# Performance work log

Measured on AMD Instinct MI355X. Metric: run time of the kernel, lower is better.

Reference implementation:

```python
import jax, jax.numpy as jnp
import numpy as np

CHANNELS = 128
HEADS = 4
R = 2
LAMBDA = 0.1


def setup_inputs() -> dict:
    key = jax.random.key(0)
    k1, k2 = jax.random.split(key)
    x = jax.random.normal(k1, (1, CHANNELS, 32, 32, 32), dtype=jnp.float32)
    # 1x1x1 Conv3d weight [3C, C] (trailing unit spatial dims dropped), fan-in scaled
    w_qkv = jax.random.normal(k2, (3 * CHANNELS, CHANNELS), dtype=jnp.float32) * (CHANNELS ** -0.5)
    return {"x": x, "w_qkv": w_qkv}


def reference(x, w_qkv):
    head_dim = CHANNELS // HEADS          # 32
    d_half = head_dim // 2                # 16
    scale = head_dim ** -0.5
    # AvgPool3d(kernel_size=1, stride=R) == strided subsampling
    xs = x[:, :, ::R, ::R, ::R]
    B, C, H, W, Z = xs.shape
    N = H * W * Z                          # 4096 tokens
    # 1x1x1 conv == pointwise channel matmul, then group channels heads-major
    qkv = jnp.einsum('oc,bchwz->bohwz', w_qkv, xs).reshape(B, HEADS, 3 * head_dim, N)
    q, k, v = jnp.split(qkv, 3, axis=2)    # each [B, h, head_dim, N]
    q1, q2 = q[:, :, :d_half, :], q[:, :, d_half:, :]
    k1, k2 = k[:, :, :d_half, :], k[:, :, d_half:, :]
    # two full score matrices [B, h, N, N] (differential attention)
    attn1 = jnp.einsum('bhdn,bhdm->bhnm', q1, k1) * scale
    attn2 = jnp.einsum('bhdn,bhdm->bhnm', q2, k2) * scale
    diff_attn = jax.nn.softmax(attn1, axis=-1) - LAMBDA * jax.nn.softmax(attn2, axis=-1)
    out = jnp.einsum('bhnm,bhdm->bhnd', diff_attn, v)  # [B, h, N, head_dim]
    # faithful to torch .view(B, -1, H, W, Z) on contiguous (h, N, head_dim) layout
    return out.reshape(B, C, H, W, Z)
```

## Files before the change

### kernel.cpp

```cpp
#include <hip/hip_runtime.h>

#define N_TOK 4096
#define NH    4

typedef __attribute__((ext_vector_type(8))) short bf16x8;
typedef __attribute__((ext_vector_type(4))) short bf16x4;
typedef __attribute__((ext_vector_type(4))) float f32x4;

static constexpr float SCALE   = 0.17677669529663687f;
static constexpr float QSCALE  = 0.25503632254435463f;
static constexpr float LAMBDA_ = 0.1f;
#define PSTRIDE 2112

__device__ __forceinline__ unsigned short bf_rne(float f) {
    unsigned u = __float_as_uint(f);
    u += 0x7FFF + ((u >> 16) & 1);
    return (unsigned short)(u >> 16);
}

__global__ __launch_bounds__(256) void qkv_kernel(
    const float* __restrict__ x, const float* __restrict__ wsrc,
    unsigned short* __restrict__ qA, unsigned short* __restrict__ kB,
    unsigned short* __restrict__ vT)
{
    __shared__ __align__(16) float xf[16][132];
    __shared__ __align__(16) unsigned short xbh[16 * 136];
    __shared__ __align__(16) unsigned short xbl[16 * 136];
    __shared__ __align__(16) unsigned short qsh[2][16][64];
    __shared__ __align__(16) unsigned short ksh[2][16][64];
    __shared__ __align__(16) unsigned short vsh[2][32][16];

    const int t  = threadIdx.x;
    const int tg = blockIdx.x >> 1;
    const int rh = blockIdx.x & 1;
    const int n0 = tg * 16;
    const int nh = n0 >> 8, nw = (n0 >> 4) & 15;
    const int xbase = nh * 2048 + nw * 64;

    #pragma unroll
    for (int k = 0; k < 4; ++k) {
        int idx = t + k * 256;
        int pair = idx & 7, ch = idx >> 3;
        float4 f4 = *(const float4*)&x[(size_t)ch * 32768 + xbase + pair * 4];
        xf[pair * 2][ch]     = f4.x;
        xf[pair * 2 + 1][ch] = f4.z;
    }
    __syncthreads();
    #pragma unroll
    for (int k = 0; k < 8; ++k) {
        int idx = t + k * 256;
        int tok = idx & 15, ch = idx >> 4;
        float f = xf[tok][ch];
        unsigned u = __float_as_uint(f);
        float lo = f - __uint_as_float(u & 0xFFFF0000u);
        xbh[tok * 136 + ch] = (unsigned short)(u >> 16);
        xbl[tok * 136 + ch] = (unsigned short)(__float_as_uint(lo) >> 16);
    }
    __syncthreads();

    const int lane = t & 63;
    const int m    = lane & 15;
    const int quad = lane >> 4;
    const int w    = t >> 6;

    bf16x8 Bh[4], Bl[4];
    #pragma unroll
    for (int s = 0; s < 4; ++s) {
        Bh[s] = *(const bf16x8*)&xbh[m * 136 + s * 32 + quad * 8];
        Bl[s] = *(const bf16x8*)&xbl[m * 136 + s * 32 + quad * 8];
    }

    #pragma unroll
    for (int rt = 0; rt < 3; ++rt) {
        const int R0 = rh * 192 + w * 48 + rt * 16;
        const int row = R0 + m;
        const int rr_row = row % 96;
        const float sc = (rr_row < 32) ? QSCALE : 1.0f;
        const float* wp = wsrc + (size_t)row * 128;
        bf16x8 Ah[4], Al[4];
        #pragma unroll
        for (int s = 0; s < 4; ++s) {
            float4 f0 = *(const float4*)(wp + s * 32 + quad * 8);
            float4 f1 = *(const float4*)(wp + s * 32 + quad * 8 + 4);
            float fv[8] = {f0.x, f0.y, f0.z, f0.w, f1.x, f1.y, f1.z, f1.w};
            #pragma unroll
            for (int j = 0; j < 8; ++j) {
                float f = fv[j] * sc;
                unsigned u = __float_as_uint(f);
                float lo = f - __uint_as_float(u & 0xFFFF0000u);
                Ah[s][j] = (short)(unsigned short)(u >> 16);
                Al[s][j] = (short)(unsigned short)(__float_as_uint(lo) >> 16);
            }
        }
        f32x4 C = {0, 0, 0, 0};
        #pragma unroll
        for (int s = 0; s < 4; ++s) {
            C = __builtin_amdgcn_mfma_f32_16x16x32_bf16(Ah[s], Bh[s], C, 0, 0, 0);
            C = __builtin_amdgcn_mfma_f32_16x16x32_bf16(Al[s], Bh[s], C, 0, 0, 0);
            C = __builtin_amdgcn_mfma_f32_16x16x32_bf16(Ah[s], Bl[s], C, 0, 0, 0);
        }
        #pragma unroll
        for (int i = 0; i < 4; ++i) {
            int R  = R0 + quad * 4 + i;
            int hh = R / 96;
            int rr = R - hh * 96;
            int hl = hh & 1;
            float f = C[i];
            if (rr < 64) {
                unsigned u = __float_as_uint(f);
                float lo = f - __uint_as_float(u & 0xFFFF0000u);
                unsigned short hi16 = (unsigned short)(u >> 16);
                unsigned short lo16 = (unsigned short)(__float_as_uint(lo) >> 16);
                int part = (rr & 31) >> 4, d = rr & 15;
                if (rr < 32) {
                    qsh[hl][m][part * 32 + d]      = hi16;
                    qsh[hl][m][part * 32 + d + 16] = lo16;
                } else {
                    ksh[hl][m][part * 32 + d]      = hi16;
                    ksh[hl][m][part * 32 + d + 16] = lo16;
                }
            } else {
                vsh[hl][rr - 64][m] = bf_rne(f);
            }
        }
    }
    __syncthreads();

    {
        int rec = t >> 3, g = t & 7;
        int hl  = rec >> 4, i = rec & 15;
        int hh  = rh * 2 + hl;
        int n   = n0 + i;
        size_t qbase = ((size_t)hh * N_TOK + n) * 64 + g * 8;
        *(uint4*)(qA + qbase) = *(const uint4*)&qsh[hl][i][g * 8];

        int tile = n >> 6, ml = n & 63;
        int kh2 = ml >> 5, mlb = (ml >> 4) & 1, mm = ml & 15;
        int f = mlb * 2 + (g >> 2), qd = g & 3;
        size_t koff = (size_t)hh * 262144 + (size_t)tile * 4096
                    + ((kh2 * 4 + f) * 64 + qd * 16 + mm) * 8;
        *(uint4*)(kB + koff) = *(const uint4*)&ksh[hl][i][g * 8];
    }
    if (t < 128) {
        int hl = t >> 6, d = (t >> 1) & 31, half = t & 1;
        int hh = rh * 2 + hl;
        int kb = (n0 >> 3) + half;
        int tile = kb >> 3, kbl = kb & 7;
        int kh2 = kbl >> 2;
        int vf  = ((kbl >> 1) & 1) * 2 + (d >> 4);
        int mm  = d & 15;
        size_t vbase = (size_t)hh * 131072 + (size_t)tile * 2048 + (kh2 * 4 + vf) * 256;
        int q0 = (kbl & 1) << 1;
        *(uint2*)(vT + vbase + (q0 * 16 + mm) * 4)       = *(const uint2*)&vsh[hl][d][half * 8];
        *(uint2*)(vT + vbase + ((q0 + 1) * 16 + mm) * 4) = *(const uint2*)&vsh[hl][d][half * 8 + 4];
    }
}

__global__ __launch_bounds__(256, 4) void flash_kernel(
    const unsigned short* __restrict__ qA, const unsigned short* __restrict__ kB,
    const unsigned short* __restrict__ vT, float* __restrict__ parts)
{
    __shared__ float Obuf[2][2][16][33];
    __shared__ float lbuf[2][2][16];

    const int t    = threadIdx.x;
    const int w    = t >> 6;
    const int lane = t & 63;
    const int m    = lane & 15;
    const int quad = lane >> 4;
    const int ks   = blockIdx.x & 1;
    const int qt   = (blockIdx.x >> 1) & 127;
    const int h    = blockIdx.x >> 8;
    const int qtile = w >> 1;
    const int kh    = w & 1;
    const int qbase = qt * 32;

    for (int i = t; i < 2112; i += 256) ((float*)Obuf)[i] = 0.f;
    if (t < 64) ((float*)lbuf)[t] = 0.f;
    __syncthreads();

    const unsigned short* qrec = qA + (size_t)(h * N_TOK + qbase + qtile * 16 + m) * 64;
    const bf16x8 zz = {0,0,0,0,0,0,0,0};
    bf16x8 Bq1h = *(const bf16x8*)(qrec + (quad & 1) * 8);
    bf16x8 Bq2h = *(const bf16x8*)(qrec + 32 + (quad & 1) * 8);
    bf16x8 Bq1l = (quad < 2) ? *(const bf16x8*)(qrec + 16 + quad * 8) : zz;
    bf16x8 Bq2l = (quad < 2) ? *(const bf16x8*)(qrec + 48 + quad * 8) : zz;

    f32x4 O1a = {0,0,0,0}, O1b = {0,0,0,0}, O2a = {0,0,0,0}, O2b = {0,0,0,0};
    float l1 = 0.f, l2 = 0.f;

    const unsigned short* kt = kB + (size_t)h * 262144 + (size_t)ks * 131072;
    const unsigned short* vt = vT + (size_t)h * 131072 + (size_t)ks * 65536;
    const int kcb = kh * 2048 + lane * 8;
    const int vcb = kh * 1024 + lane * 4;

    bf16x8 Ka0, Ka1, Ka2, Ka3, Kb0, Kb1, Kb2, Kb3;
    bf16x4 Va0, Va1, Va2, Va3, Vb0, Vb1, Vb2, Vb3;

#define LOADSET(K0, K1, K2, K3, V0, V1, V2, V3, TILE)                          \
    {                                                                          \
        const unsigned short* kp = kt + (size_t)(TILE) * 4096 + kcb;           \
        const unsigned short* vp = vt + (size_t)(TILE) * 2048 + vcb;           \
        K0 = *(const bf16x8*)(kp);                                             \
        K1 = *(const bf16x8*)(kp + 512);                                       \
        K2 = *(const bf16x8*)(kp + 1024);                                      \
        K3 = *(const bf16x8*)(kp + 1536);                                      \
        V0 = *(const bf16x4*)(vp);                                             \
        V1 = *(const bf16x4*)(vp + 256);                                       \
        V2 = *(const bf16x4*)(vp + 512);                                       \
        V3 = *(const bf16x4*)(vp + 768);                                       \
    }

    auto compute = [&](bf16x8 K1_0, bf16x8 K2_0, bf16x8 K1_1, bf16x8 K2_1,
                       bf16x4 V00, bf16x4 V10, bf16x4 V01, bf16x4 V11) {
        __builtin_amdgcn_s_setprio(1);
        f32x4 sA1 = {0,0,0,0}, sA2 = {0,0,0,0};
        f32x4 sB1 = {0,0,0,0}, sB2 = {0,0,0,0};
        sA1 = __builtin_amdgcn_mfma_f32_16x16x32_bf16(K1_0, Bq1h, sA1, 0, 0, 0);
        sB1 = __builtin_amdgcn_mfma_f32_16x16x32_bf16(K1_1, Bq1h, sB1, 0, 0, 0);
        sA1 = __builtin_amdgcn_mfma_f32_16x16x32_bf16(K1_0, Bq1l, sA1, 0, 0, 0);
        sB1 = __builtin_amdgcn_mfma_f32_16x16x32_bf16(K1_1, Bq1l, sB1, 0, 0, 0);
        sA2 = __builtin_amdgcn_mfma_f32_16x16x32_bf16(K2_0, Bq2h, sA2, 0, 0, 0);
        sB2 = __builtin_amdgcn_mfma_f32_16x16x32_bf16(K2_1, Bq2h, sB2, 0, 0, 0);
        sA2 = __builtin_amdgcn_mfma_f32_16x16x32_bf16(K2_0, Bq2l, sA2, 0, 0, 0);
        sB2 = __builtin_amdgcn_mfma_f32_16x16x32_bf16(K2_1, Bq2l, sB2, 0, 0, 0);

        float pa0 = __builtin_amdgcn_exp2f(sA1[0]), pa1 = __builtin_amdgcn_exp2f(sA1[1]);
        float pa2 = __builtin_amdgcn_exp2f(sA1[2]), pa3 = __builtin_amdgcn_exp2f(sA1[3]);
        float pb0 = __builtin_amdgcn_exp2f(sB1[0]), pb1 = __builtin_amdgcn_exp2f(sB1[1]);
        float pb2 = __builtin_amdgcn_exp2f(sB1[2]), pb3 = __builtin_amdgcn_exp2f(sB1[3]);
        float qa0 = __builtin_amdgcn_exp2f(sA2[0]), qa1 = __builtin_amdgcn_exp2f(sA2[1]);
        float qa2 = __builtin_amdgcn_exp2f(sA2[2]), qa3 = __builtin_amdgcn_exp2f(sA2[3]);
        float qb0 = __builtin_amdgcn_exp2f(sB2[0]), qb1 = __builtin_amdgcn_exp2f(sB2[1]);
        float qb2 = __builtin_amdgcn_exp2f(sB2[2]), qb3 = __builtin_amdgcn_exp2f(sB2[3]);
        l1 += (pa0 + pa1) + (pa2 + pa3) + (pb0 + pb1) + (pb2 + pb3);
        l2 += (qa0 + qa1) + (qa2 + qa3) + (qb0 + qb1) + (qb2 + qb3);
        union { unsigned u[2]; bf16x4 v; } cA1, cB1, cA2, cB2;
        cA1.u[0] = __builtin_amdgcn_perm(__float_as_uint(pa1), __float_as_uint(pa0), 0x07060302u);
        cA1.u[1] = __builtin_amdgcn_perm(__float_as_uint(pa3), __float_as_uint(pa2), 0x07060302u);
        cB1.u[0] = __builtin_amdgcn_perm(__float_as_uint(pb1), __float_as_uint(pb0), 0x07060302u);
        cB1.u[1] = __builtin_amdgcn_perm(__float_as_uint(pb3), __float_as_uint(pb2), 0x07060302u);
        cA2.u[0] = __builtin_amdgcn_perm(__float_as_uint(qa1), __float_as_uint(qa0), 0x07060302u);
        cA2.u[1] = __builtin_amdgcn_perm(__float_as_uint(qa3), __float_as_uint(qa2), 0x07060302u);
        cB2.u[0] = __builtin_amdgcn_perm(__float_as_uint(qb1), __float_as_uint(qb0), 0x07060302u);
        cB2.u[1] = __builtin_amdgcn_perm(__float_as_uint(qb3), __float_as_uint(qb2), 0x07060302u);

        O1a = __builtin_amdgcn_mfma_f32_16x16x16bf16_1k(cA1.v, V00, O1a, 0, 0, 0);
        O1b = __builtin_amdgcn_mfma_f32_16x16x16bf16_1k(cA1.v, V10, O1b, 0, 0, 0);
        O2a = __builtin_amdgcn_mfma_f32_16x16x16bf16_1k(cA2.v, V00, O2a, 0, 0, 0);
        O2b = __builtin_amdgcn_mfma_f32_16x16x16bf16_1k(cA2.v, V10, O2b, 0, 0, 0);
        O1a = __builtin_amdgcn_mfma_f32_16x16x16bf16_1k(cB1.v, V01, O1a, 0, 0, 0);
        O1b = __builtin_amdgcn_mfma_f32_16x16x16bf16_1k(cB1.v, V11, O1b, 0, 0, 0);
        O2a = __builtin_amdgcn_mfma_f32_16x16x16bf16_1k(cB2.v, V01, O2a, 0, 0, 0);
        O2b = __builtin_amdgcn_mfma_f32_16x16x16bf16_1k(cB2.v, V11, O2b, 0, 0, 0);
        __builtin_amdgcn_s_setprio(0);
    };

    LOADSET(Ka0, Ka1, Ka2, Ka3, Va0, Va1, Va2, Va3, 0);
    for (int tile = 0; tile < 32; tile += 2) {
        LOADSET(Kb0, Kb1, Kb2, Kb3, Vb0, Vb1, Vb2, Vb3, tile + 1);
        compute(Ka0, Ka1, Ka2, Ka3, Va0, Va1, Va2, Va3);
        if (tile + 2 < 32)
            LOADSET(Ka0, Ka1, Ka2, Ka3, Va0, Va1, Va2, Va3, tile + 2);
        compute(Kb0, Kb1, Kb2, Kb3, Vb0, Vb1, Vb2, Vb3);
    }
#undef LOADSET

    l1 += __shfl_xor(l1, 16, 64); l1 += __shfl_xor(l1, 32, 64);
    l2 += __shfl_xor(l2, 16, 64); l2 += __shfl_xor(l2, 32, 64);
    if (lane < 16) {
        atomicAdd(&lbuf[qtile][0][m], l1);
        atomicAdd(&lbuf[qtile][1][m], l2);
    }
    #pragma unroll
    for (int i = 0; i < 4; ++i) {
        int r = quad * 4 + i;
        atomicAdd(&Obuf[qtile][0][r][m],      O1a[i]);
        atomicAdd(&Obuf[qtile][0][r][16 + m], O1b[i]);
        atomicAdd(&Obuf[qtile][1][r][m],      O2a[i]);
        atomicAdd(&Obuf[qtile][1][r][16 + m], O2b[i]);
    }
    __syncthreads();

    float* dst = parts + (size_t)((h * 128 + qt) * 2 + ks) * PSTRIDE;
    for (int i = t; i < 1024; i += 256) {
        int r = i >> 5, d = i & 31;
        int qtl = r >> 4, rl = r & 15;
        dst[i]        = Obuf[qtl][0][rl][d];
        dst[1024 + i] = Obuf[qtl][1][rl][d];
    }
    if (t < 32) {
        int qtl = t >> 4, rl = t & 15;
        dst[2048 + t] = lbuf[qtl][0][rl];
        dst[2080 + t] = lbuf[qtl][1][rl];
    }
}

__global__ __launch_bounds__(256) void merge_kernel(
    const float* __restrict__ parts, float* __restrict__ out)
{
    int idx = blockIdx.x * 256 + threadIdx.x;
    int d4 = (idx & 7) * 4;
    int row = idx >> 3;
    int h = row >> 12, n = row & 4095;
    int qt = n >> 5, r = n & 31;
    const float* p0 = parts + (size_t)((h * 128 + qt) * 2) * PSTRIDE;
    const float* p1 = p0 + PSTRIDE;
    float4 a1 = *(const float4*)(p0 + r * 32 + d4);
    float4 b1 = *(const float4*)(p1 + r * 32 + d4);
    float4 a2 = *(const float4*)(p0 + 1024 + r * 32 + d4);
    float4 b2 = *(const float4*)(p1 + 1024 + r * 32 + d4);
    float l1 = p0[2048 + r] + p1[2048 + r];
    float l2 = p0[2080 + r] + p1[2080 + r];
    float4 o;
    o.x = (a1.x + b1.x) / l1 - LAMBDA_ * ((a2.x + b2.x) / l2);
    o.y = (a1.y + b1.y) / l1 - LAMBDA_ * ((a2.y + b2.y) / l2);
    o.z = (a1.z + b1.z) / l1 - LAMBDA_ * ((a2.z + b2.z) / l2);
    o.w = (a1.w + b1.w) / l1 - LAMBDA_ * ((a2.w + b2.w) / l2);
    *(float4*)(out + (size_t)idx * 4) = o;
}

extern "C" void kernel_launch(void* const* d_in, const int* in_sizes, int n_in,
                              void* d_out, int out_size, void* d_ws, size_t ws_size,
                              hipStream_t stream) {
    const float* x = (const float*)d_in[0];
    const float* w = (const float*)d_in[1];
    float* out = (float*)d_out;

    unsigned short* qA = (unsigned short*)d_ws;
    unsigned short* kB = qA + (size_t)NH * N_TOK * 64;
    unsigned short* vT = kB + (size_t)NH * N_TOK * 64;
    float* parts = (float*)(vT + (size_t)NH * 32 * N_TOK);

    qkv_kernel<<<512, 256, 0, stream>>>(x, w, qA, kB, vT);
    flash_kernel<<<1024, 256, 0, stream>>>(qA, kB, vT, parts);
    merge_kernel<<<512, 256, 0, stream>>>(parts, out);
}
```

Baseline: 120.7 us.

## Software-pipeline QK^T of the next tile with softmax and PV of the current

Splits the per-tile work into separate QK^T and exp/PV phases and staggers them. The score MFMAs for tile i+1 are issued before the exp2, pack and PV MFMAs of tile i, with K loads running one further tile ahead of V loads. The goal is to hide MFMA result latency and the exp/pack VALU work behind independent matrix ops. In exchange it keeps two sets of score accumulators live, and the launch bound no longer requests 4 blocks per CU. The compiler can therefore use more registers, which may lower occupancy.

```diff
diff --git a/kernel.cpp b/kernel.cpp
--- a/kernel.cpp
+++ b/kernel.cpp
@@ -156,7 +156,7 @@
     }
 }
 
-__global__ __launch_bounds__(256, 4) void flash_kernel(
+__global__ __launch_bounds__(256) void flash_kernel(
     const unsigned short* __restrict__ qA, const unsigned short* __restrict__ kB,
     const unsigned short* __restrict__ vT, float* __restrict__ parts)
 {
@@ -194,77 +194,90 @@
     const int kcb = kh * 2048 + lane * 8;
     const int vcb = kh * 1024 + lane * 4;
 
-    bf16x8 Ka0, Ka1, Ka2, Ka3, Kb0, Kb1, Kb2, Kb3;
-    bf16x4 Va0, Va1, Va2, Va3, Vb0, Vb1, Vb2, Vb3;
-
-#define LOADSET(K0, K1, K2, K3, V0, V1, V2, V3, TILE)                          \
-    {                                                                          \
+    bf16x8 K00, K01, K02, K03, K10, K11, K12, K13;
+    bf16x4 V00_, V01_, V02_, V03_, V10_, V11_, V12_, V13_;
+    f32x4 S0A1, S0B1, S0A2, S0B2, S1A1, S1B1, S1A2, S1B2;
+
+#define LOADK(KS, TILE) {                                                      \
         const unsigned short* kp = kt + (size_t)(TILE) * 4096 + kcb;           \
+        KS##0 = *(const bf16x8*)(kp);                                          \
+        KS##1 = *(const bf16x8*)(kp + 512);                                    \
+        KS##2 = *(const bf16x8*)(kp + 1024);                                   \
+        KS##3 = *(const bf16x8*)(kp + 1536);                                   \
+    }
+#define LOADV(VS, TILE) {                                                      \
         const unsigned short* vp = vt + (size_t)(TILE) * 2048 + vcb;           \
-        K0 = *(const bf16x8*)(kp);                                             \
-        K1 = *(const bf16x8*)(kp + 512);                                       \
-        K2 = *(const bf16x8*)(kp + 1024);                                      \
-        K3 = *(const bf16x8*)(kp + 1536);                                      \
-        V0 = *(const bf16x4*)(vp);                                             \
-        V1 = *(const bf16x4*)(vp + 256);                                       \
-        V2 = *(const bf16x4*)(vp + 512);                                       \
-        V3 = *(const bf16x4*)(vp + 768);                                       \
-    }
-
-    auto compute = [&](bf16x8 K1_0, bf16x8 K2_0, bf16x8 K1_1, bf16x8 K2_1,
-                       bf16x4 V00, bf16x4 V10, bf16x4 V01, bf16x4 V11) {
-        __builtin_amdgcn_s_setprio(1);
-        f32x4 sA1 = {0,0,0,0}, sA2 = {0,0,0,0};
-        f32x4 sB1 = {0,0,0,0}, sB2 = {0,0,0,0};
-        sA1 = __builtin_amdgcn_mfma_f32_16x16x32_bf16(K1_0, Bq1h, sA1, 0, 0, 0);
-        sB1 = __builtin_amdgcn_mfma_f32_16x16x32_bf16(K1_1, Bq1h, sB1, 0, 0, 0);
-        sA1 = __builtin_amdgcn_mfma_f32_16x16x32_bf16(K1_0, Bq1l, sA1, 0, 0, 0);
-        sB1 = __builtin_amdgcn_mfma_f32_16x16x32_bf16(K1_1, Bq1l, sB1, 0, 0, 0);
-        sA2 = __builtin_amdgcn_mfma_f32_16x16x32_bf16(K2_0, Bq2h, sA2, 0, 0, 0);
-        sB2 = __builtin_amdgcn_mfma_f32_16x16x32_bf16(K2_1, Bq2h, sB2, 0, 0, 0);
-        sA2 = __builtin_amdgcn_mfma_f32_16x16x32_bf16(K2_0, Bq2l, sA2, 0, 0, 0);
-        sB2 = __builtin_amdgcn_mfma_f32_16x16x32_bf16(K2_1, Bq2l, sB2, 0, 0, 0);
-
-        float pa0 = __builtin_amdgcn_exp2f(sA1[0]), pa1 = __builtin_amdgcn_exp2f(sA1[1]);
-        float pa2 = __builtin_amdgcn_exp2f(sA1[2]), pa3 = __builtin_amdgcn_exp2f(sA1[3]);
-        float pb0 = __builtin_amdgcn_exp2f(sB1[0]), pb1 = __builtin_amdgcn_exp2f(sB1[1]);
-        float pb2 = __builtin_amdgcn_exp2f(sB1[2]), pb3 = __builtin_amdgcn_exp2f(sB1[3]);
-        float qa0 = __builtin_amdgcn_exp2f(sA2[0]), qa1 = __builtin_amdgcn_exp2f(sA2[1]);
-        float qa2 = __builtin_amdgcn_exp2f(sA2[2]), qa3 = __builtin_amdgcn_exp2f(sA2[3]);
-        float qb0 = __builtin_amdgcn_exp2f(sB2[0]), qb1 = __builtin_amdgcn_exp2f(sB2[1]);
-        float qb2 = __builtin_amdgcn_exp2f(sB2[2]), qb3 = __builtin_amdgcn_exp2f(sB2[3]);
-        l1 += (pa0 + pa1) + (pa2 + pa3) + (pb0 + pb1) + (pb2 + pb3);
-        l2 += (qa0 + qa1) + (qa2 + qa3) + (qb0 + qb1) + (qb2 + qb3);
-        union { unsigned u[2]; bf16x4 v; } cA1, cB1, cA2, cB2;
-        cA1.u[0] = __builtin_amdgcn_perm(__float_as_uint(pa1), __float_as_uint(pa0), 0x07060302u);
-        cA1.u[1] = __builtin_amdgcn_perm(__float_as_uint(pa3), __float_as_uint(pa2), 0x07060302u);
-        cB1.u[0] = __builtin_amdgcn_perm(__float_as_uint(pb1), __float_as_uint(pb0), 0x07060302u);
-        cB1.u[1] = __builtin_amdgcn_perm(__float_as_uint(pb3), __float_as_uint(pb2), 0x07060302u);
-        cA2.u[0] = __builtin_amdgcn_perm(__float_as_uint(qa1), __float_as_uint(qa0), 0x07060302u);
-        cA2.u[1] = __builtin_amdgcn_perm(__float_as_uint(qa3), __float_as_uint(qa2), 0x07060302u);
-        cB2.u[0] = __builtin_amdgcn_perm(__float_as_uint(qb1), __float_as_uint(qb0), 0x07060302u);
-        cB2.u[1] = __builtin_amdgcn_perm(__float_as_uint(qb3), __float_as_uint(qb2), 0x07060302u);
-
-        O1a = __builtin_amdgcn_mfma_f32_16x16x16bf16_1k(cA1.v, V00, O1a, 0, 0, 0);
-        O1b = __builtin_amdgcn_mfma_f32_16x16x16bf16_1k(cA1.v, V10, O1b, 0, 0, 0);
-        O2a = __builtin_amdgcn_mfma_f32_16x16x16bf16_1k(cA2.v, V00, O2a, 0, 0, 0);
-        O2b = __builtin_amdgcn_mfma_f32_16x16x16bf16_1k(cA2.v, V10, O2b, 0, 0, 0);
-        O1a = __builtin_amdgcn_mfma_f32_16x16x16bf16_1k(cB1.v, V01, O1a, 0, 0, 0);
-        O1b = __builtin_amdgcn_mfma_f32_16x16x16bf16_1k(cB1.v, V11, O1b, 0, 0, 0);
-        O2a = __builtin_amdgcn_mfma_f32_16x16x16bf16_1k(cB2.v, V01, O2a, 0, 0, 0);
-        O2b = __builtin_amdgcn_mfma_f32_16x16x16bf16_1k(cB2.v, V11, O2b, 0, 0, 0);
-        __builtin_amdgcn_s_setprio(0);
-    };
-
-    LOADSET(Ka0, Ka1, Ka2, Ka3, Va0, Va1, Va2, Va3, 0);
-    for (int tile = 0; tile < 32; tile += 2) {
-        LOADSET(Kb0, Kb1, Kb2, Kb3, Vb0, Vb1, Vb2, Vb3, tile + 1);
-        compute(Ka0, Ka1, Ka2, Ka3, Va0, Va1, Va2, Va3);
-        if (tile + 2 < 32)
-            LOADSET(Ka0, Ka1, Ka2, Ka3, Va0, Va1, Va2, Va3, tile + 2);
-        compute(Kb0, Kb1, Kb2, Kb3, Vb0, Vb1, Vb2, Vb3);
-    }
-#undef LOADSET
+        VS##0_ = *(const bf16x4*)(vp);                                         \
+        VS##1_ = *(const bf16x4*)(vp + 256);                                   \
+        VS##2_ = *(const bf16x4*)(vp + 512);                                   \
+        VS##3_ = *(const bf16x4*)(vp + 768);                                   \
+    }
+#define QKPH(SS, KS) {                                                         \
+        __builtin_amdgcn_s_setprio(1);                                         \
+        SS##A1 = (f32x4){0,0,0,0}; SS##B1 = (f32x4){0,0,0,0};                  \
+        SS##A2 = (f32x4){0,0,0,0}; SS##B2 = (f32x4){0,0,0,0};                  \
+        SS##A1 = __builtin_amdgcn_mfma_f32_16x16x32_bf16(KS##0, Bq1h, SS##A1, 0, 0, 0); \
+        SS##B1 = __builtin_amdgcn_mfma_f32_16x16x32_bf16(KS##2, Bq1h, SS##B1, 0, 0, 0); \
+        SS##A1 = __builtin_amdgcn_mfma_f32_16x16x32_bf16(KS##0, Bq1l, SS##A1, 0, 0, 0); \
+        SS##B1 = __builtin_amdgcn_mfma_f32_16x16x32_bf16(KS##2, Bq1l, SS##B1, 0, 0, 0); \
+        SS##A2 = __builtin_amdgcn_mfma_f32_16x16x32_bf16(KS##1, Bq2h, SS##A2, 0, 0, 0); \
+        SS##B2 = __builtin_amdgcn_mfma_f32_16x16x32_bf16(KS##3, Bq2h, SS##B2, 0, 0, 0); \
+        SS##A2 = __builtin_amdgcn_mfma_f32_16x16x32_bf16(KS##1, Bq2l, SS##A2, 0, 0, 0); \
+        SS##B2 = __builtin_amdgcn_mfma_f32_16x16x32_bf16(KS##3, Bq2l, SS##B2, 0, 0, 0); \
+    }
+#define PVPH(SS, VS) {                                                         \
+        float pa0 = __builtin_amdgcn_exp2f(SS##A1[0]), pa1 = __builtin_amdgcn_exp2f(SS##A1[1]); \
+        float pa2 = __builtin_amdgcn_exp2f(SS##A1[2]), pa3 = __builtin_amdgcn_exp2f(SS##A1[3]); \
+        float pb0 = __builtin_amdgcn_exp2f(SS##B1[0]), pb1 = __builtin_amdgcn_exp2f(SS##B1[1]); \
+        float pb2 = __builtin_amdgcn_exp2f(SS##B1[2]), pb3 = __builtin_amdgcn_exp2f(SS##B1[3]); \
+        float qa0 = __builtin_amdgcn_exp2f(SS##A2[0]), qa1 = __builtin_amdgcn_exp2f(SS##A2[1]); \
+        float qa2 = __builtin_amdgcn_exp2f(SS##A2[2]), qa3 = __builtin_amdgcn_exp2f(SS##A2[3]); \
+        float qb0 = __builtin_amdgcn_exp2f(SS##B2[0]), qb1 = __builtin_amdgcn_exp2f(SS##B2[1]); \
+        float qb2 = __builtin_amdgcn_exp2f(SS##B2[2]), qb3 = __builtin_amdgcn_exp2f(SS##B2[3]); \
+        l1 += (pa0 + pa1) + (pa2 + pa3) + (pb0 + pb1) + (pb2 + pb3);           \
+        l2 += (qa0 + qa1) + (qa2 + qa3) + (qb0 + qb1) + (qb2 + qb3);           \
+        union { unsigned u[2]; bf16x4 v; } cA1, cB1, cA2, cB2;                 \
+        cA1.u[0] = __builtin_amdgcn_perm(__float_as_uint(pa1), __float_as_uint(pa0), 0x07060302u); \
+        cA1.u[1] = __builtin_amdgcn_perm(__float_as_uint(pa3), __float_as_uint(pa2), 0x07060302u); \
+        cB1.u[0] = __builtin_amdgcn_perm(__float_as_uint(pb1), __float_as_uint(pb0), 0x07060302u); \
+        cB1.u[1] = __builtin_amdgcn_perm(__float_as_uint(pb3), __float_as_uint(pb2), 0x07060302u); \
+        cA2.u[0] = __builtin_amdgcn_perm(__float_as_uint(qa1), __float_as_uint(qa0), 0x07060302u); \
+        cA2.u[1] = __builtin_amdgcn_perm(__float_as_uint(qa3), __float_as_uint(qa2), 0x07060302u); \
+        cB2.u[0] = __builtin_amdgcn_perm(__float_as_uint(qb1), __float_as_uint(qb0), 0x07060302u); \
+        cB2.u[1] = __builtin_amdgcn_perm(__float_as_uint(qb3), __float_as_uint(qb2), 0x07060302u); \
+        O1a = __builtin_amdgcn_mfma_f32_16x16x16bf16_1k(cA1.v, VS##0_, O1a, 0, 0, 0); \
+        O1b = __builtin_amdgcn_mfma_f32_16x16x16bf16_1k(cA1.v, VS##1_, O1b, 0, 0, 0); \
+        O2a = __builtin_amdgcn_mfma_f32_16x16x16bf16_1k(cA2.v, VS##0_, O2a, 0, 0, 0); \
+        O2b = __builtin_amdgcn_mfma_f32_16x16x16bf16_1k(cA2.v, VS##1_, O2b, 0, 0, 0); \
+        O1a = __builtin_amdgcn_mfma_f32_16x16x16bf16_1k(cB1.v, VS##2_, O1a, 0, 0, 0); \
+        O1b = __builtin_amdgcn_mfma_f32_16x16x16bf16_1k(cB1.v, VS##3_, O1b, 0, 0, 0); \
+        O2a = __builtin_amdgcn_mfma_f32_16x16x16bf16_1k(cB2.v, VS##2_, O2a, 0, 0, 0); \
+        O2b = __builtin_amdgcn_mfma_f32_16x16x16bf16_1k(cB2.v, VS##3_, O2b, 0, 0, 0); \
+        __builtin_amdgcn_s_setprio(0);                                         \
+    }
+
+    LOADK(K0, 0); LOADK(K1, 1); LOADV(V0, 0);
+    QKPH(S0, K0);
+
+    for (int tl = 0; tl < 30; tl += 2) {
+        LOADK(K0, tl + 2);
+        LOADV(V1, tl + 1);
+        QKPH(S1, K1);
+        PVPH(S0, V0);
+        LOADK(K1, tl + 3);
+        LOADV(V0, tl + 2);
+        QKPH(S0, K0);
+        PVPH(S1, V1);
+    }
+    LOADV(V1, 31);
+    QKPH(S1, K1);
+    PVPH(S0, V0);
+    PVPH(S1, V1);
+
+#undef LOADK
+#undef LOADV
+#undef QKPH
+#undef PVPH
 
     l1 += __shfl_xor(l1, 16, 64); l1 += __shfl_xor(l1, 32, 64);
     l2 += __shfl_xor(l2, 16, 64); l2 += __shfl_xor(l2, 32, 64);
```

Result: slower. 128.3 us (+6.3%).
